# Optimization experiments

Measured on AMD Instinct MI355X. Metric: run time of the kernel, lower is better.

The kernel has to match this reference:

```python
import jax, jax.numpy as jnp
import numpy as np

D_MODEL = 2048
N_HEADS = 16
DH = D_MODEL // N_HEADS
B, S, S_CACHE = 2, 1024, 1024


def setup_inputs() -> dict:
    key = jax.random.key(0)
    ks = jax.random.split(key, 5)
    x = jax.random.normal(ks[0], (B, S, D_MODEL), dtype=jnp.float32)
    k_cache = jax.random.normal(ks[1], (B, N_HEADS, S_CACHE, DH), dtype=jnp.float32)
    v_cache = jax.random.normal(ks[2], (B, N_HEADS, S_CACHE, DH), dtype=jnp.float32)
    qkv = 0.01 * jax.random.normal(ks[3], (3 * D_MODEL, D_MODEL), dtype=jnp.float32)
    wo = 0.01 * jax.random.normal(ks[4], (D_MODEL, D_MODEL), dtype=jnp.float32)
    return {"x": x, "k_cache": k_cache, "v_cache": v_cache,
            "qkv": qkv, "wo": wo, "past_length": S_CACHE}


def reference(x, k_cache, v_cache, qkv, wo, past_length):
    Bn, Sn, D = x.shape
    H, dh = N_HEADS, D // N_HEADS
    # Fused QKV projection: (B,S,3D)
    QKV = jnp.einsum('bsd,ed->bse', x, qkv)
    Q, K, V = jnp.split(QKV, 3, axis=-1)
    # (B,H,S,dh)
    q = Q.reshape(Bn, Sn, H, dh).transpose(0, 2, 1, 3)
    k = K.reshape(Bn, Sn, H, dh).transpose(0, 2, 1, 3)
    v = V.reshape(Bn, Sn, H, dh).transpose(0, 2, 1, 3)
    # KV-cache concat along sequence dim
    k_full = jnp.concatenate([k_cache, k], axis=2)
    v_full = jnp.concatenate([v_cache, v], axis=2)
    S_full = k_full.shape[2]
    # Causal mask shifted by past_length: query i attends to keys j <= i + past_length
    rows = jnp.arange(Sn)[:, None]
    cols = jnp.arange(S_full)[None, :]
    allowed = cols <= rows + past_length  # (S, S_full)
    scale = 1.0 / jnp.sqrt(jnp.asarray(dh, x.dtype))
    scores = jnp.einsum('bhqd,bhkd->bhqk', q, k_full) * scale
    scores = jnp.where(allowed[None, None], scores, jnp.finfo(scores.dtype).min)
    attn = jax.nn.softmax(scores, axis=-1)
    ctx = jnp.einsum('bhqk,bhkd->bhqd', attn, v_full)
    out = ctx.transpose(0, 2, 1, 3).reshape(Bn, Sn, D)
    out = jnp.einsum('bsd,ed->bse', out, wo)
    return out, k_full, v_full
```

## Files before the change

### kernel.cpp

```cpp
#include <hip/hip_runtime.h>
#include <cstdint>

#define HB 2
#define HS 1024
#define HSF 2048
#define HH 16
#define HDH 128
#define HD 2048
#define HD3 6144
#define HM 2048

typedef __attribute__((ext_vector_type(8))) short bf16x8;
typedef __attribute__((ext_vector_type(4))) float f32x4;
typedef __attribute__((ext_vector_type(16))) float f32x16;
typedef unsigned short u16;
typedef unsigned int u32;

__device__ __forceinline__ u16 f2b(float f) {
    union { float f; u32 u; } v; v.f = f;
    u32 u = v.u;
    return (u16)((u + 0x7FFFu + ((u >> 16) & 1u)) >> 16);
}
__device__ __forceinline__ float b2f(u16 h) {
    union { u32 u; float f; } v; v.u = ((u32)h) << 16; return v.f;
}

__device__ __forceinline__ f32x4 mfma16x16(bf16x8 a, bf16x8 b, f32x4 c) {
    return __builtin_amdgcn_mfma_f32_16x16x32_bf16(a, b, c, 0, 0, 0);
}
__device__ __forceinline__ f32x16 mfma32x32(bf16x8 a, bf16x8 b, f32x16 c) {
    return __builtin_amdgcn_mfma_f32_32x32x16_bf16(a, b, c, 0, 0, 0);
}
__device__ __forceinline__ void pl32swap(u32 &a, u32 &b) {
    asm volatile("v_permlane32_swap_b32 %0, %1" : "+v"(a), "+v"(b));
}

#define GLD16(gp, lp) __builtin_amdgcn_global_load_lds( \
    (__attribute__((address_space(1))) void*)(gp), \
    (__attribute__((address_space(3))) void*)(lp), 16, 0, 0)

__global__ __launch_bounds__(256) void k_prep(
    const float* __restrict__ x,  u16* __restrict__ xb,  int n0,
    const float* __restrict__ qkv, u16* __restrict__ qkvb, int n1,
    const float* __restrict__ wo,  u16* __restrict__ wob, int n2,
    const float* __restrict__ kc, const float* __restrict__ vc,
    float* __restrict__ kf, float* __restrict__ vf,
    u16* __restrict__ kb, u16* __restrict__ vt)
{
    const int bid = blockIdx.x;
    const int tid = threadIdx.x;
    if (bid < 512) {
        __shared__ u16 Lt[128 * 66];
        int bh = bid >> 4, st = (bid & 15) << 6;
        size_t cbase = (size_t)bh * (HS * HDH) + (size_t)st * HDH;
        size_t fbase = (size_t)bh * (HSF * HDH) + (size_t)st * HDH;
        #pragma unroll
        for (int i = 0; i < 8; ++i) {
            int ci = i * 256 + tid;
            float4 kv = ((const float4*)(kc + cbase))[ci];
            ((float4*)(kf + fbase))[ci] = kv;
            ushort4 k4;
            k4.x = f2b(kv.x); k4.y = f2b(kv.y); k4.z = f2b(kv.z); k4.w = f2b(kv.w);
            ((ushort4*)(kb + fbase))[ci] = k4;
        }
        #pragma unroll
        for (int i = 0; i < 8; ++i) {
            int ci = i * 256 + tid;
            int r = ci >> 5, c = ci & 31;
            float4 vv = ((const float4*)(vc + cbase))[ci];
            ((float4*)(vf + fbase))[ci] = vv;
            int dh = c * 4;
            Lt[(dh + 0) * 66 + r] = f2b(vv.x);
            Lt[(dh + 1) * 66 + r] = f2b(vv.y);
            Lt[(dh + 2) * 66 + r] = f2b(vv.z);
            Lt[(dh + 3) * 66 + r] = f2b(vv.w);
        }
        __syncthreads();
        u16* vtb = vt + (size_t)bh * (HDH * HSF) + st;
        #pragma unroll
        for (int i = 0; i < 4; ++i) {
            int ci = i * 256 + tid;
            int dh = ci >> 3, cs = (ci & 7) * 8;
            const u16* lr = &Lt[dh * 66 + cs];
            ushort4 lo, hi2;
            lo.x = lr[0]; lo.y = lr[1]; lo.z = lr[2]; lo.w = lr[3];
            hi2.x = lr[4]; hi2.y = lr[5]; hi2.z = lr[6]; hi2.w = lr[7];
            u16* dst = vtb + (size_t)dh * HSF + cs;
            *(ushort4*)dst = lo;
            *(ushort4*)(dst + 4) = hi2;
        }
    } else {
        int i = (bid - 512) * 256 + tid;
        const int st_ = ((int)gridDim.x - 512) * 256;
        const int nt = n0 + n1 + n2;
        for (; i < nt; i += st_) {
            const float* s; u16* d; int j = i;
            if (j < n0) { s = x; d = xb; }
            else if (j < n0 + n1) { j -= n0; s = qkv; d = qkvb; }
            else { j -= n0 + n1; s = wo; d = wob; }
            float4 v = ((const float4*)s)[j];
            ushort4 o;
            o.x = f2b(v.x); o.y = f2b(v.y); o.z = f2b(v.z); o.w = f2b(v.w);
            ((ushort4*)d)[j] = o;
        }
    }
}

__global__ __launch_bounds__(256, 2) void k_gemm_qkv(
    const u16* __restrict__ A, const u16* __restrict__ Bw, int K,
    u16* __restrict__ qb, float* __restrict__ kf, float* __restrict__ vf,
    u16* __restrict__ kb, u16* __restrict__ vt)
{
    __shared__ __align__(16) u16 SH[16384];
    u16* As = SH;
    u16* Bs = SH + 8192;
    const int tid = threadIdx.x;
    const int w = tid >> 6, lane = tid & 63;
    const int wm = w >> 1, wn = w & 1;
    const int lcol = lane & 15, lhi = lane >> 4;

    const int nb = (int)gridDim.x, per = nb >> 3;
    const int bf = (int)blockIdx.x;
    const int t = (bf & 7) * per + (bf >> 3);
    const int m0 = (t & 15) * 128, n0 = (t >> 4) * 128;

    const int srow = lane >> 2;
    const int scol = ((lane & 3) ^ ((lane >> 4) & 2)) * 8;
    const int c0 = w * 2, c1 = w * 2 + 1;
    const u16* Ag0 = A + (size_t)(m0 + c0 * 16 + srow) * K + scol;
    const u16* Ag1 = A + (size_t)(m0 + c1 * 16 + srow) * K + scol;
    const u16* Bg0 = Bw + (size_t)(n0 + c0 * 16 + srow) * K + scol;
    const u16* Bg1 = Bw + (size_t)(n0 + c1 * 16 + srow) * K + scol;

    const int lx = lhi ^ ((lcol >> 2) & 2);

    f32x4 acc[4][4] = {};

    GLD16(Ag0, &As[c0 * 512]);
    GLD16(Ag1, &As[c1 * 512]);
    GLD16(Bg0, &Bs[c0 * 512]);
    GLD16(Bg1, &Bs[c1 * 512]);
    __syncthreads();

    int cur = 0;
    for (int k0 = 0; k0 < K; k0 += 32) {
        if (k0 + 32 < K) {
            int nb_ = (cur ^ 1) * 4096;
            GLD16(Ag0 + k0 + 32, &As[nb_ + c0 * 512]);
            GLD16(Ag1 + k0 + 32, &As[nb_ + c1 * 512]);
            GLD16(Bg0 + k0 + 32, &Bs[nb_ + c0 * 512]);
            GLD16(Bg1 + k0 + 32, &Bs[nb_ + c1 * 512]);
        }
        const int cb = cur * 4096;
        bf16x8 af[4], bfr[4];
        #pragma unroll
        for (int i = 0; i < 4; ++i)
            af[i] = *(const bf16x8*)&As[cb + (wm * 64 + i * 16 + lcol) * 32 + lx * 8];
        #pragma unroll
        for (int i = 0; i < 4; ++i)
            bfr[i] = *(const bf16x8*)&Bs[cb + (wn * 64 + i * 16 + lcol) * 32 + lx * 8];
        __builtin_amdgcn_s_setprio(1);
        #pragma unroll
        for (int i = 0; i < 4; ++i)
            #pragma unroll
            for (int j = 0; j < 4; ++j)
                acc[i][j] = mfma16x16(af[i], bfr[j], acc[i][j]);
        __builtin_amdgcn_s_setprio(0);
        __syncthreads();
        cur ^= 1;
    }

    const int bsec = n0 >> 11;
    if (bsec == 2) {
        u16* T = SH;
        #pragma unroll
        for (int i = 0; i < 4; ++i) {
          #pragma unroll
          for (int j = 0; j < 4; ++j) {
            #pragma unroll
            for (int r = 0; r < 4; ++r) {
                int sl = wm * 64 + i * 16 + lhi * 4 + r;
                int dl = wn * 64 + j * 16 + lcol;
                int m = m0 + sl, n = n0 + dl;
                float v = acc[i][j][r];
                int b = m >> 10, s = m & 1023;
                int e = n & 2047;
                int h = e >> 7, dh = e & 127;
                int bh = b * HH + h;
                vf[((size_t)bh * HSF + HS + s) * HDH + dh] = v;
                T[dl * 128 + (sl ^ ((dl & 15) << 3))] = f2b(v);
            }
          }
        }
        __syncthreads();
        const int b2 = m0 >> 10, s0 = m0 & 1023;
        const int hh = (n0 & 2047) >> 7;
        const int bh2 = b2 * HH + hh;
        u16* vtb = vt + (size_t)(bh2 * HDH) * HSF + HS + s0;
        #pragma unroll
        for (int it = 0; it < 8; ++it) {
            int ci = it * 256 + tid;
            int dl = ci >> 4, ch = ci & 15;
            const u16* lr = &T[dl * 128 + ((ch * 8) ^ ((dl & 15) << 3))];
            ushort4 lo = *(const ushort4*)lr;
            ushort4 hi2 = *(const ushort4*)(lr + 4);
            u16* dst = vtb + (size_t)dl * HSF + ch * 8;
            *(ushort4*)dst = lo;
            *(ushort4*)(dst + 4) = hi2;
        }
    } else {
        #pragma unroll
        for (int i = 0; i < 4; ++i) {
          #pragma unroll
          for (int j = 0; j < 4; ++j) {
            #pragma unroll
            for (int r = 0; r < 4; ++r) {
                int m = m0 + wm * 64 + i * 16 + lhi * 4 + r;
                int n = n0 + wn * 64 + j * 16 + lcol;
                float v = acc[i][j][r];
                int b = m >> 10, s = m & 1023;
                int e = n & 2047;
                int h = e >> 7, dh = e & 127;
                int bh = b * HH + h;
                if (bsec == 0) {
                    qb[((size_t)bh * HS + s) * HDH + dh] = f2b(v * 0.12751742f);
                } else {
                    size_t idx = ((size_t)bh * HSF + HS + s) * HDH + dh;
                    kf[idx] = v; kb[idx] = f2b(v);
                }
            }
          }
        }
    }
}

__global__ __launch_bounds__(256, 4) void k_gemm_out(
    const u16* __restrict__ A, const u16* __restrict__ Bw, int K,
    float* __restrict__ outf)
{
    __shared__ __align__(16) u16 As[2 * 128 * 32];
    __shared__ __align__(16) u16 Bs[2 * 64 * 32];
    const int tid = threadIdx.x;
    const int w = tid >> 6, lane = tid & 63;
    const int wm = w >> 1, wn = w & 1;
    const int lcol = lane & 15, lhi = lane >> 4;

    const int nb = (int)gridDim.x, per = nb >> 3;
    const int bf = (int)blockIdx.x;
    const int t = (bf & 7) * per + (bf >> 3);
    const int m0 = (t & 15) * 128, n0 = (t >> 4) * 64;

    const int srow = lane >> 2;
    const int scol = ((lane & 3) ^ ((lane >> 4) & 2)) * 8;
    const int c0 = w * 2, c1 = w * 2 + 1;
    const u16* Ag0 = A + (size_t)(m0 + c0 * 16 + srow) * K + scol;
    const u16* Ag1 = A + (size_t)(m0 + c1 * 16 + srow) * K + scol;
    const u16* Bg0 = Bw + (size_t)(n0 + w * 16 + srow) * K + scol;

    const int lx = lhi ^ ((lcol >> 2) & 2);

    f32x4 acc[4][2] = {};

    GLD16(Ag0, &As[c0 * 512]);
    GLD16(Ag1, &As[c1 * 512]);
    GLD16(Bg0, &Bs[w * 512]);
    __syncthreads();

    int cur = 0;
    for (int k0 = 0; k0 < K; k0 += 32) {
        if (k0 + 32 < K) {
            GLD16(Ag0 + k0 + 32, &As[(cur ^ 1) * 4096 + c0 * 512]);
            GLD16(Ag1 + k0 + 32, &As[(cur ^ 1) * 4096 + c1 * 512]);
            GLD16(Bg0 + k0 + 32, &Bs[(cur ^ 1) * 2048 + w * 512]);
        }
        const int ca = cur * 4096, cb2 = cur * 2048;
        bf16x8 af[4], bfr[2];
        #pragma unroll
        for (int i = 0; i < 4; ++i)
            af[i] = *(const bf16x8*)&As[ca + (wm * 64 + i * 16 + lcol) * 32 + lx * 8];
        #pragma unroll
        for (int j = 0; j < 2; ++j)
            bfr[j] = *(const bf16x8*)&Bs[cb2 + (wn * 32 + j * 16 + lcol) * 32 + lx * 8];
        __builtin_amdgcn_s_setprio(1);
        #pragma unroll
        for (int i = 0; i < 4; ++i)
            #pragma unroll
            for (int j = 0; j < 2; ++j)
                acc[i][j] = mfma16x16(af[i], bfr[j], acc[i][j]);
        __builtin_amdgcn_s_setprio(0);
        __syncthreads();
        cur ^= 1;
    }

    #pragma unroll
    for (int i = 0; i < 4; ++i)
      #pragma unroll
      for (int j = 0; j < 2; ++j)
        #pragma unroll
        for (int r = 0; r < 4; ++r) {
            int m = m0 + wm * 64 + i * 16 + lhi * 4 + r;
            int n = n0 + wn * 32 + j * 16 + lcol;
            outf[(size_t)m * HD + n] = acc[i][j][r];
        }
}

__global__ __launch_bounds__(256, 3) void k_attn(
    const u16* __restrict__ qb, const u16* __restrict__ kb,
    const u16* __restrict__ vt, u16* __restrict__ pO,
    float* __restrict__ pM, float* __restrict__ pL,
    const int* __restrict__ plp)
{
    __shared__ __align__(16) u16 Ks[64 * 128];
    __shared__ __align__(16) u16 Vs[128 * 64];

    const int past = *plp;
    const int tid = threadIdx.x, w = tid >> 6, lane = tid & 63;
    const int l31 = lane & 31, hi = lane >> 5;

    const int bid = blockIdx.x;
    const int orig = (bid & 7) * 96 + (bid >> 3);
    const int split = orig % 3;
    const int rest = orig / 3;
    const int qblk = rest & 7;
    const int bh = rest >> 3;
    const int q0b = qblk * 128;
    const int q0 = q0b + w * 32;
    const int q = q0 + l31;

    const u16* qx = qb + (size_t)bh * HS * HDH;
    const u16* kx = kb + (size_t)bh * HSF * HDH;
    const u16* vx = vt + (size_t)bh * HDH * HSF;

    bf16x8 qf[8];
    #pragma unroll
    for (int c = 0; c < 8; ++c)
        qf[c] = *(const bf16x8*)&qx[(size_t)q * HDH + c * 16 + hi * 8];

    const int krow0 = w * 16 + (lane >> 4);
    const int kchunk = lane & 15;
    const int vrow0 = w * 32 + (lane >> 3);
    const int vchunk = lane & 7;

    f32x16 o[4] = {};
    float mr = -3e38f, lr = 0.f;

    int nkt = (q0b + 128 + past + 63) >> 6;
    if (nkt > HSF / 64) nkt = HSF / 64;
    const int t0 = (split * nkt) / 3;
    const int t1 = ((split + 1) * nkt) / 3;

    for (int kt = t0; kt < t1; ++kt) {
        const int j0 = kt * 64;
        __syncthreads();
        #pragma unroll
        for (int i = 0; i < 4; ++i) {
            int rk = krow0 + 4 * i;
            GLD16(kx + (size_t)(j0 + rk) * HDH + ((kchunk ^ (rk & 7)) * 8),
                  Ks + w * 2048 + i * 512);
            int rv = vrow0 + 8 * i;
            GLD16(vx + (size_t)rv * HSF + j0 + ((vchunk ^ (rv & 7)) * 8),
                  Vs + w * 2048 + i * 512);
        }
        __syncthreads();

        if (j0 > q0 + 31 + past) continue;

        const char* ksb = (const char*)Ks;
        f32x16 sf0 = {}, sf1 = {};
        const int sw = l31 & 7;
        __builtin_amdgcn_s_setprio(1);
        #pragma unroll
        for (int c = 0; c < 8; ++c) {
            int ch = ((c * 2 + hi) ^ sw) * 16;
            bf16x8 ak0 = *(const bf16x8*)(ksb + l31 * 256 + ch);
            sf0 = mfma32x32(ak0, qf[c], sf0);
            bf16x8 ak1 = *(const bf16x8*)(ksb + (32 + l31) * 256 + ch);
            sf1 = mfma32x32(ak1, qf[c], sf1);
        }
        __builtin_amdgcn_s_setprio(0);

        if (j0 + 63 > q0 + past) {
            #pragma unroll
            for (int r = 0; r < 16; ++r) {
                int ko = (r & 3) + 8 * (r >> 2) + 4 * hi;
                if (j0 + ko > q + past)      sf0[r] = -3e38f;
                if (j0 + 32 + ko > q + past) sf1[r] = -3e38f;
            }
        }
        float pmax = -3e38f;
        #pragma unroll
        for (int r = 0; r < 16; ++r)
            pmax = fmaxf(pmax, fmaxf(sf0[r], sf1[r]));
        pmax = fmaxf(pmax, __shfl_xor(pmax, 32, 64));
        if (!__all((int)(pmax <= mr + 8.f))) {
            float mnew = fmaxf(mr, pmax);
            float alpha = exp2f(mr - mnew);
            mr = mnew;
            lr *= alpha;
            #pragma unroll
            for (int dt = 0; dt < 4; ++dt) o[dt] *= alpha;
        }
        float ps = 0.f;
        #pragma unroll
        for (int r = 0; r < 16; ++r) {
            sf0[r] = exp2f(sf0[r] - mr);
            sf1[r] = exp2f(sf1[r] - mr);
            ps += sf0[r] + sf1[r];
        }
        ps += __shfl_xor(ps, 32, 64);
        lr += ps;

        u32 wA[8], wB[8];
        #pragma unroll
        for (int g = 0; g < 4; ++g) {
            asm("v_cvt_pk_bf16_f32 %0, %1, %2" : "=v"(wA[2*g])   : "v"(sf0[4*g+0]), "v"(sf0[4*g+1]));
            asm("v_cvt_pk_bf16_f32 %0, %1, %2" : "=v"(wA[2*g+1]) : "v"(sf0[4*g+2]), "v"(sf0[4*g+3]));
            asm("v_cvt_pk_bf16_f32 %0, %1, %2" : "=v"(wB[2*g])   : "v"(sf1[4*g+0]), "v"(sf1[4*g+1]));
            asm("v_cvt_pk_bf16_f32 %0, %1, %2" : "=v"(wB[2*g+1]) : "v"(sf1[4*g+2]), "v"(sf1[4*g+3]));
        }
        pl32swap(wA[0], wA[2]); pl32swap(wA[1], wA[3]);
        pl32swap(wA[4], wA[6]); pl32swap(wA[5], wA[7]);
        pl32swap(wB[0], wB[2]); pl32swap(wB[1], wB[3]);
        pl32swap(wB[4], wB[6]); pl32swap(wB[5], wB[7]);
        union uf { u32 u[4]; bf16x8 v; };
        uf pf0, pf1, pf2, pf3;
        pf0.u[0]=wA[0]; pf0.u[1]=wA[1]; pf0.u[2]=wA[2]; pf0.u[3]=wA[3];
        pf1.u[0]=wA[4]; pf1.u[1]=wA[5]; pf1.u[2]=wA[6]; pf1.u[3]=wA[7];
        pf2.u[0]=wB[0]; pf2.u[1]=wB[1]; pf2.u[2]=wB[2]; pf2.u[3]=wB[3];
        pf3.u[0]=wB[4]; pf3.u[1]=wB[5]; pf3.u[2]=wB[6]; pf3.u[3]=wB[7];

        const char* vsb = (const char*)Vs;
        __builtin_amdgcn_s_setprio(1);
        #pragma unroll
        for (int dt = 0; dt < 4; ++dt) {
            int rb = (dt * 32 + l31) * 128;
            bf16x8 av0 = *(const bf16x8*)(vsb + rb + (((0 + hi) ^ sw) * 16));
            o[dt] = mfma32x32(av0, pf0.v, o[dt]);
            bf16x8 av1 = *(const bf16x8*)(vsb + rb + (((2 + hi) ^ sw) * 16));
            o[dt] = mfma32x32(av1, pf1.v, o[dt]);
            bf16x8 av2 = *(const bf16x8*)(vsb + rb + (((4 + hi) ^ sw) * 16));
            o[dt] = mfma32x32(av2, pf2.v, o[dt]);
            bf16x8 av3 = *(const bf16x8*)(vsb + rb + (((6 + hi) ^ sw) * 16));
            o[dt] = mfma32x32(av3, pf3.v, o[dt]);
        }
        __builtin_amdgcn_s_setprio(0);
    }

    const int qg = bh * HS + q;
    if (hi == 0) {
        pM[split * 32768 + qg] = mr;
        pL[split * 32768 + qg] = lr;
    }
    u16* prow = pO + ((size_t)split * 32768 + qg) * 128;
    #pragma unroll
    for (int dt = 0; dt < 4; ++dt)
        #pragma unroll
        for (int g = 0; g < 4; ++g) {
            ushort4 wv;
            wv.x = f2b(o[dt][4*g+0]);
            wv.y = f2b(o[dt][4*g+1]);
            wv.z = f2b(o[dt][4*g+2]);
            wv.w = f2b(o[dt][4*g+3]);
            *(ushort4*)(prow + dt * 32 + 8 * g + 4 * hi) = wv;
        }
}

__global__ __launch_bounds__(256) void k_combine(
    const u16* __restrict__ pO, const float* __restrict__ pM,
    const float* __restrict__ pL, u16* __restrict__ ctx)
{
    int t = blockIdx.x * 256 + threadIdx.x;
    int qg = t >> 5;
    int d4 = (t & 31) << 2;
    float m0 = pM[qg], m1 = pM[32768 + qg], m2 = pM[65536 + qg];
    float l0 = pL[qg], l1 = pL[32768 + qg], l2 = pL[65536 + qg];
    float M = fmaxf(fmaxf(m0, m1), m2);
    float a0 = exp2f(m0 - M), a1 = exp2f(m1 - M), a2 = exp2f(m2 - M);
    float inv = 1.f / (a0 * l0 + a1 * l1 + a2 * l2);
    a0 *= inv; a1 *= inv; a2 *= inv;
    ushort4 v0 = *(const ushort4*)(pO + (size_t)qg * 128 + d4);
    ushort4 v1 = *(const ushort4*)(pO + ((size_t)32768 + qg) * 128 + d4);
    ushort4 v2 = *(const ushort4*)(pO + ((size_t)65536 + qg) * 128 + d4);
    int bh = qg >> 10, qq = qg & 1023;
    int b = bh >> 4, hh = bh & 15;
    u16* crow = ctx + ((size_t)(b * HS + qq)) * HD + hh * HDH + d4;
    ushort4 wv;
    wv.x = f2b(a0 * b2f(v0.x) + a1 * b2f(v1.x) + a2 * b2f(v2.x));
    wv.y = f2b(a0 * b2f(v0.y) + a1 * b2f(v1.y) + a2 * b2f(v2.y));
    wv.z = f2b(a0 * b2f(v0.z) + a1 * b2f(v1.z) + a2 * b2f(v2.z));
    wv.w = f2b(a0 * b2f(v0.w) + a1 * b2f(v1.w) + a2 * b2f(v2.w));
    *(ushort4*)crow = wv;
}

extern "C" void kernel_launch(void* const* d_in, const int* in_sizes, int n_in,
                              void* d_out, int out_size, void* d_ws, size_t ws_size,
                              hipStream_t stream) {
    const float* x   = (const float*)d_in[0];
    const float* kc  = (const float*)d_in[1];
    const float* vc  = (const float*)d_in[2];
    const float* qkv = (const float*)d_in[3];
    const float* wo  = (const float*)d_in[4];
    const int* plp   = (const int*)d_in[5];

    float* out = (float*)d_out;
    float* kf  = out + (size_t)HB * HS * HD;
    float* vf  = kf + (size_t)HB * HH * HSF * HDH;

    char* ws = (char*)d_ws;
    size_t o1 = (size_t)HM * HD * 2;
    size_t o2 = o1 + (size_t)HD3 * HD * 2;
    size_t o3 = o2 + (size_t)HD * HD * 2;
    size_t o4 = o3 + (size_t)HB * HH * HS * HDH * 2;
    size_t o5 = o4 + (size_t)HB * HH * HSF * HDH * 2;
    size_t o6 = o5 + (size_t)HB * HH * HSF * HDH * 2;
    u16* xb   = (u16*)(ws);
    u16* qkvb = (u16*)(ws + o1);
    u16* wob  = (u16*)(ws + o2);
    u16* qb   = (u16*)(ws + o3);
    u16* kb   = (u16*)(ws + o4);
    u16* vt   = (u16*)(ws + o5);
    u16* ctxb = (u16*)(ws + o6);
    u16* pO   = (u16*)ws;
    float* pM = (float*)(ws + (size_t)3 * 32768 * 128 * 2);
    float* pL = (float*)(ws + (size_t)3 * 32768 * 128 * 2 + 393216);

    k_prep<<<2048, 256, 0, stream>>>(x, xb, HM * HD / 4,
                                     qkv, qkvb, HD3 * HD / 4,
                                     wo, wob, HD * HD / 4,
                                     kc, vc, kf, vf, kb, vt);

    k_gemm_qkv<<<768, 256, 0, stream>>>(
        xb, qkvb, HD, qb, kf, vf, kb, vt);

    k_attn<<<768, 256, 0, stream>>>(qb, kb, vt, pO, pM, pL, plp);
    k_combine<<<4096, 256, 0, stream>>>(pO, pM, pL, ctxb);

    k_gemm_out<<<512, 256, 0, stream>>>(ctxb, wob, HD, out);
}
```

Measured before the change: 195.8 us.

## Enlarge QKV GEMM tiles to 256x256 with 512-thread blocks and BK=64

Restructures the QKV projection GEMM from 128x128 tiles with 256 threads and BK=32 into 256x256 tiles with 8 waves, BK=64 and a 128 KB double-buffered LDS with XOR swizzle. Each wave now computes a 128x64 sub-tile with 32 accumulators. The goal is higher arithmetic intensity and fewer global loads per FLOP. In exchange the grid shrinks from 768 to 192 blocks, which is fewer than two waves per CU on a 256-CU part and leaves an occupancy of one block per CU, so load balance and latency hiding may suffer. The V transpose epilogue is rewritten to span two heads per tile.

```diff
diff --git a/kernel.cpp b/kernel.cpp
--- a/kernel.cpp
+++ b/kernel.cpp
@@ -106,66 +106,74 @@
     }
 }
 
-__global__ __launch_bounds__(256, 2) void k_gemm_qkv(
+__global__ __launch_bounds__(512, 1) void k_gemm_qkv(
     const u16* __restrict__ A, const u16* __restrict__ Bw, int K,
     u16* __restrict__ qb, float* __restrict__ kf, float* __restrict__ vf,
     u16* __restrict__ kb, u16* __restrict__ vt)
 {
-    __shared__ __align__(16) u16 SH[16384];
-    u16* As = SH;
-    u16* Bs = SH + 8192;
+    __shared__ __align__(16) u16 SH[65536];
     const int tid = threadIdx.x;
     const int w = tid >> 6, lane = tid & 63;
-    const int wm = w >> 1, wn = w & 1;
+    const int wr = w >> 2, wc = w & 3;
     const int lcol = lane & 15, lhi = lane >> 4;
-
-    const int nb = (int)gridDim.x, per = nb >> 3;
+    const int NT = 32;
+
     const int bf = (int)blockIdx.x;
-    const int t = (bf & 7) * per + (bf >> 3);
-    const int m0 = (t & 15) * 128, n0 = (t >> 4) * 128;
-
-    const int srow = lane >> 2;
-    const int scol = ((lane & 3) ^ ((lane >> 4) & 2)) * 8;
-    const int c0 = w * 2, c1 = w * 2 + 1;
-    const u16* Ag0 = A + (size_t)(m0 + c0 * 16 + srow) * K + scol;
-    const u16* Ag1 = A + (size_t)(m0 + c1 * 16 + srow) * K + scol;
-    const u16* Bg0 = Bw + (size_t)(n0 + c0 * 16 + srow) * K + scol;
-    const u16* Bg1 = Bw + (size_t)(n0 + c1 * 16 + srow) * K + scol;
-
-    const int lx = lhi ^ ((lcol >> 2) & 2);
-
-    f32x4 acc[4][4] = {};
-
-    GLD16(Ag0, &As[c0 * 512]);
-    GLD16(Ag1, &As[c1 * 512]);
-    GLD16(Bg0, &Bs[c0 * 512]);
-    GLD16(Bg1, &Bs[c1 * 512]);
+    const int t = (bf & 7) * 24 + (bf >> 3);
+    const int m0 = (t & 7) * 256, n0 = (t >> 3) * 256;
+
+    const int srow = tid >> 3;
+    const int schunk = tid & 7;
+
+    auto STAGE = [&](int buf, int kt) {
+        #pragma unroll
+        for (int L = 0; L < 4; ++L) {
+            int row = L * 64 + srow;
+            int cs = (schunk ^ (row & 7)) * 8;
+            GLD16(A + (size_t)(m0 + row) * K + kt * 64 + cs,
+                  &SH[buf * 32768 + L * 4096 + w * 512]);
+        }
+        #pragma unroll
+        for (int L = 0; L < 4; ++L) {
+            int row = L * 64 + srow;
+            int cs = (schunk ^ (row & 7)) * 8;
+            GLD16(Bw + (size_t)(n0 + row) * K + kt * 64 + cs,
+                  &SH[buf * 32768 + 16384 + L * 4096 + w * 512]);
+        }
+    };
+
+    f32x4 acc[8][4] = {};
+
+    STAGE(0, 0);
     __syncthreads();
 
     int cur = 0;
-    for (int k0 = 0; k0 < K; k0 += 32) {
-        if (k0 + 32 < K) {
-            int nb_ = (cur ^ 1) * 4096;
-            GLD16(Ag0 + k0 + 32, &As[nb_ + c0 * 512]);
-            GLD16(Ag1 + k0 + 32, &As[nb_ + c1 * 512]);
-            GLD16(Bg0 + k0 + 32, &Bs[nb_ + c0 * 512]);
-            GLD16(Bg1 + k0 + 32, &Bs[nb_ + c1 * 512]);
-        }
-        const int cb = cur * 4096;
-        bf16x8 af[4], bfr[4];
-        #pragma unroll
-        for (int i = 0; i < 4; ++i)
-            af[i] = *(const bf16x8*)&As[cb + (wm * 64 + i * 16 + lcol) * 32 + lx * 8];
-        #pragma unroll
-        for (int i = 0; i < 4; ++i)
-            bfr[i] = *(const bf16x8*)&Bs[cb + (wn * 64 + i * 16 + lcol) * 32 + lx * 8];
-        __builtin_amdgcn_s_setprio(1);
-        #pragma unroll
-        for (int i = 0; i < 4; ++i)
-            #pragma unroll
-            for (int j = 0; j < 4; ++j)
-                acc[i][j] = mfma16x16(af[i], bfr[j], acc[i][j]);
-        __builtin_amdgcn_s_setprio(0);
+    for (int kt = 0; kt < NT; ++kt) {
+        if (kt + 1 < NT) STAGE(cur ^ 1, kt + 1);
+        const int ab = cur * 32768, bb = cur * 32768 + 16384;
+        #pragma unroll
+        for (int kk = 0; kk < 2; ++kk) {
+            bf16x8 af[8], bfr[4];
+            #pragma unroll
+            for (int i = 0; i < 8; ++i) {
+                int r = wr * 128 + i * 16 + lcol;
+                int ch = (kk * 4 + lhi) ^ (r & 7);
+                af[i] = *(const bf16x8*)&SH[ab + r * 64 + ch * 8];
+            }
+            #pragma unroll
+            for (int j = 0; j < 4; ++j) {
+                int r = wc * 64 + j * 16 + lcol;
+                int ch = (kk * 4 + lhi) ^ (r & 7);
+                bfr[j] = *(const bf16x8*)&SH[bb + r * 64 + ch * 8];
+            }
+            __builtin_amdgcn_s_setprio(1);
+            #pragma unroll
+            for (int i = 0; i < 8; ++i)
+                #pragma unroll
+                for (int j = 0; j < 4; ++j)
+                    acc[i][j] = mfma16x16(af[i], bfr[j], acc[i][j]);
+            __builtin_amdgcn_s_setprio(0);
+        }
         __syncthreads();
         cur ^= 1;
     }
@@ -174,13 +182,13 @@
     if (bsec == 2) {
         u16* T = SH;
         #pragma unroll
-        for (int i = 0; i < 4; ++i) {
+        for (int i = 0; i < 8; ++i) {
           #pragma unroll
           for (int j = 0; j < 4; ++j) {
             #pragma unroll
             for (int r = 0; r < 4; ++r) {
-                int sl = wm * 64 + i * 16 + lhi * 4 + r;
-                int dl = wn * 64 + j * 16 + lcol;
+                int sl = wr * 128 + i * 16 + lhi * 4 + r;
+                int dl = wc * 64 + j * 16 + lcol;
                 int m = m0 + sl, n = n0 + dl;
                 float v = acc[i][j][r];
                 int b = m >> 10, s = m & 1023;
@@ -188,35 +196,34 @@
                 int h = e >> 7, dh = e & 127;
                 int bh = b * HH + h;
                 vf[((size_t)bh * HSF + HS + s) * HDH + dh] = v;
-                T[dl * 128 + (sl ^ ((dl & 15) << 3))] = f2b(v);
+                T[dl * 256 + (sl ^ ((dl & 31) << 3))] = f2b(v);
             }
           }
         }
         __syncthreads();
         const int b2 = m0 >> 10, s0 = m0 & 1023;
-        const int hh = (n0 & 2047) >> 7;
-        const int bh2 = b2 * HH + hh;
-        u16* vtb = vt + (size_t)(bh2 * HDH) * HSF + HS + s0;
-        #pragma unroll
-        for (int it = 0; it < 8; ++it) {
-            int ci = it * 256 + tid;
-            int dl = ci >> 4, ch = ci & 15;
-            const u16* lr = &T[dl * 128 + ((ch * 8) ^ ((dl & 15) << 3))];
+        #pragma unroll
+        for (int it = 0; it < 16; ++it) {
+            int ci = it * 512 + tid;
+            int dl = ci >> 5, cs = (ci & 31) * 8;
+            const u16* lr = &T[dl * 256 + (cs ^ ((dl & 31) << 3))];
             ushort4 lo = *(const ushort4*)lr;
             ushort4 hi2 = *(const ushort4*)(lr + 4);
-            u16* dst = vtb + (size_t)dl * HSF + ch * 8;
+            int e = (n0 + dl) & 2047;
+            int hh = e >> 7, dh = e & 127;
+            u16* dst = vt + ((size_t)(b2 * HH + hh) * HDH + dh) * HSF + HS + s0 + cs;
             *(ushort4*)dst = lo;
             *(ushort4*)(dst + 4) = hi2;
         }
     } else {
         #pragma unroll
-        for (int i = 0; i < 4; ++i) {
+        for (int i = 0; i < 8; ++i) {
           #pragma unroll
           for (int j = 0; j < 4; ++j) {
             #pragma unroll
             for (int r = 0; r < 4; ++r) {
-                int m = m0 + wm * 64 + i * 16 + lhi * 4 + r;
-                int n = n0 + wn * 64 + j * 16 + lcol;
+                int m = m0 + wr * 128 + i * 16 + lhi * 4 + r;
+                int n = n0 + wc * 64 + j * 16 + lcol;
                 float v = acc[i][j][r];
                 int b = m >> 10, s = m & 1023;
                 int e = n & 2047;
@@ -529,7 +536,7 @@
                                      wo, wob, HD * HD / 4,
                                      kc, vc, kf, vf, kb, vt);
 
-    k_gemm_qkv<<<768, 256, 0, stream>>>(
+    k_gemm_qkv<<<192, 512, 0, stream>>>(
         xb, qkvb, HD, qb, kf, vf, kb, vt);
 
     k_attn<<<768, 256, 0, stream>>>(qb, kb, vt, pO, pM, pL, plp);
```

Result: no change. 193.7 us (-1.1%).
